# Performance work log

Measured on AMD Instinct MI355X. Metric: run time of the kernel, lower is better.

Reference implementation:

```python
import jax, jax.numpy as jnp
import numpy as np

BN_EPS = 1e-5

def _proj(x, w):
    # 1x1x1 conv, bias=False: pure channel contraction. x: [B,C,T,H,W], w: [O,C]
    return jnp.einsum('bcthw,oc->bothw', x, w)

def _maxpool222(x):
    # MaxPool3d(kernel=2, stride=2); dims are divisible by 2.
    B, C, T, H, W = x.shape
    return x.reshape(B, C, T // 2, 2, H // 2, 2, W // 2, 2).max(axis=(3, 5, 7))

def setup_inputs() -> dict:
    key = jax.random.key(0)
    ks = jax.random.split(key, 5)
    C, Ci = 256, 128
    x = jax.random.normal(ks[0], (4, C, 16, 28, 28), dtype=jnp.float32)
    sc = 1.0 / np.sqrt(C)
    theta_w = jax.random.normal(ks[1], (Ci, C), dtype=jnp.float32) * sc
    phi_w = jax.random.normal(ks[2], (Ci, C), dtype=jnp.float32) * sc
    g_w = jax.random.normal(ks[3], (Ci, C), dtype=jnp.float32) * sc
    z_w = jax.random.normal(ks[4], (C, Ci), dtype=jnp.float32) * (1.0 / np.sqrt(Ci))
    bn_gamma = jnp.ones((C,), dtype=jnp.float32)
    bn_beta = jnp.zeros((C,), dtype=jnp.float32)
    return {"x": x, "theta_w": theta_w, "phi_w": phi_w, "g_w": g_w,
            "z_w": z_w, "bn_gamma": bn_gamma, "bn_beta": bn_beta}

def reference(x, theta_w, phi_w, g_w, z_w, bn_gamma, bn_beta):
    B, C, T, H, W = x.shape
    Ci = theta_w.shape[0]
    N = T * H * W
    theta = _proj(x, theta_w).reshape(B, Ci, N)          # [B,Ci,N]
    phi = _maxpool222(_proj(x, phi_w))                   # [B,Ci,T/2,H/2,W/2]
    g = _maxpool222(_proj(x, g_w))
    Np = phi.shape[2] * phi.shape[3] * phi.shape[4]
    phi = phi.reshape(B, Ci, Np)                         # [B,Ci,Np]
    g = g.reshape(B, Ci, Np)
    attn = jnp.einsum('bcn,bcm->bnm', theta, phi)        # [B,N,Np]
    attn = jax.nn.softmax(attn, axis=-1)
    y = jnp.einsum('bnm,bcm->bcn', attn, g)              # [B,Ci,N]
    y = y.reshape(B, Ci, T, H, W)
    z = _proj(y, z_w)                                    # [B,C,T,H,W]
    # BatchNorm3d in training mode: batch stats over (B,T,H,W), biased var
    mean = z.mean(axis=(0, 2, 3, 4), keepdims=True)
    var = z.var(axis=(0, 2, 3, 4), keepdims=True)
    zn = (z - mean) * jax.lax.rsqrt(var + BN_EPS)
    zn = zn * bn_gamma[None, :, None, None, None] + bn_beta[None, :, None, None, None]
    return x + zn
```

## Files before the change

### kernel.cpp

```cpp
#include <hip/hip_runtime.h>
#include <stdint.h>

#define B_   4
#define C_   256
#define CI_  128
#define T_   16
#define H_   28
#define W_   28
#define HW_  784
#define N_   12544
#define TP_  8
#define HP_  14
#define WP_  14
#define NP_  1568
#define NP2_ 1600
#define NT_  196
#define NT2_ 98
#define NBLK_ 784
#define NBLK2_ 392
#define KVB_ 32
#define NKT_ 49

typedef __attribute__((ext_vector_type(8))) __bf16 bf16x8;
typedef __attribute__((ext_vector_type(4))) float  f32x4;

#define MFMA(a,b,c) __builtin_amdgcn_mfma_f32_16x16x32_bf16(a,b,c,0,0,0)

__device__ __forceinline__ void split_bf16(float f, __bf16& hi, __bf16& lo){
  hi = (__bf16)f;
  lo = (__bf16)(f - (float)hi);
}

__device__ __forceinline__ uint32_t pack2(float a, float b){
  union { __bf16 h; unsigned short s; } ua, ub;
  ua.h = (__bf16)a; ub.h = (__bf16)b;
  return (uint32_t)ua.s | ((uint32_t)ub.s << 16);
}

__device__ __forceinline__ void gload_lds16(const void* g, void* l){
  __builtin_amdgcn_global_load_lds((const __attribute__((address_space(1))) void*)g,
                                   (__attribute__((address_space(3))) void*)l, 16, 0, 0);
}

__global__ __launch_bounds__(256) void k_wconv(const float* __restrict__ wt, const float* __restrict__ wp,
                       const float* __restrict__ wg, const float* __restrict__ zw,
                       __bf16* __restrict__ wth, __bf16* __restrict__ wtl,
                       __bf16* __restrict__ wph, __bf16* __restrict__ wpl,
                       __bf16* __restrict__ wgh, __bf16* __restrict__ wgl,
                       __bf16* __restrict__ zwh, __bf16* __restrict__ zwl){
  int i = blockIdx.x*256 + threadIdx.x;
  if (i < 32768){
    __bf16 h, lo;
    split_bf16(wt[i], h, lo); wth[i]=h; wtl[i]=lo;
    split_bf16(wp[i], h, lo); wph[i]=h; wpl[i]=lo;
    split_bf16(wg[i], h, lo); wgh[i]=h; wgl[i]=lo;
    split_bf16(zw[i], h, lo); zwh[i]=h; zwl[i]=lo;
  }
}

__global__ __launch_bounds__(256,4) void k_proj3(const float* __restrict__ x,
                        const __bf16* __restrict__ wth, const __bf16* __restrict__ wtl,
                        const __bf16* __restrict__ wph, const __bf16* __restrict__ wpl,
                        const __bf16* __restrict__ wgh, const __bf16* __restrict__ wgl,
                        __bf16* __restrict__ th_hi, __bf16* __restrict__ th_lo,
                        float* __restrict__ phf32, __bf16* __restrict__ ggf){
  __shared__ char wbuf[2][16384];
  int wg = blockIdx.x;
  int nt = wg % NT_; int b = wg/NT_;
  int n0 = nt*64;
  int tid = threadIdx.x; int w = tid>>6; int l = tid&63; int lr = l&15; int lg = l>>4;
  int nrow = 16*w + lr;
  const float* xb = x + (size_t)b*C_*N_ + (n0 + nrow);
  bf16x8 Ah[8], Al[8];
  #pragma unroll
  for (int ks=0; ks<8; ++ks){
    #pragma unroll
    for (int j=0;j<8;++j){
      float v = xb[(size_t)(32*ks + 8*lg + j)*N_];
      __bf16 hi, lo; split_bf16(v, hi, lo);
      Ah[ks][j] = hi; Al[ks][j] = lo;
    }
  }
  int sp_part[4]; int sp_rowc[4]; int sp_off[4];
  #pragma unroll
  for (int i=0;i<4;++i){
    int p = i*4096 + tid*16;
    sp_part[i] = p>>13;
    int row = (p>>9)&15;
    int colb = p & 511;
    sp_rowc[i] = row*C_ + ((colb ^ ((row&7)<<4)) >> 1);
    sp_off[i] = i*4096 + w*1024;
  }
  #pragma unroll
  for (int i=0;i<4;++i){
    const __bf16* src = (sp_part[i] ? wtl : wth) + sp_rowc[i];
    gload_lds16(src, &wbuf[0][sp_off[i]]);
  }
  __syncthreads();

  size_t obase = ((size_t)(b*N_ + n0))*CI_;
  int cur = 0;
  for (int pair=0; pair<24; ++pair){
    int p = pair>>3, ot = pair&7;
    if (pair < 23){
      int pn = pair+1, p2 = pn>>3, ot2 = pn&7;
      const __bf16* bh = (p2==0) ? wth : ((p2==1) ? wph : wgh);
      const __bf16* bl = (p2==0) ? wtl : ((p2==1) ? wpl : wgl);
      #pragma unroll
      for (int i=0;i<4;++i){
        const __bf16* src = (sp_part[i] ? bl : bh) + (size_t)(16*ot2)*C_ + sp_rowc[i];
        gload_lds16(src, &wbuf[cur^1][sp_off[i]]);
      }
    }
    const char* wb = wbuf[cur];
    f32x4 aHH={0.f,0.f,0.f,0.f}, aLH={0.f,0.f,0.f,0.f}, aHL={0.f,0.f,0.f,0.f};
    int swz = (lr&7)<<4;
    #pragma unroll
    for (int ks=0; ks<8; ++ks){
      int off = lr*512 + ((ks*64 + lg*16) ^ swz);
      bf16x8 Bh = *(const bf16x8*)(wb + off);
      bf16x8 Bl = *(const bf16x8*)(wb + 8192 + off);
      aHH = MFMA(Ah[ks], Bh, aHH);
      aLH = MFMA(Al[ks], Bh, aLH);
      aHL = MFMA(Ah[ks], Bl, aHL);
    }
    f32x4 acc = aHH + aLH + aHL;
    if (p == 0){
      #pragma unroll
      for (int r=0;r<4;++r){
        int n = 16*w + 4*lg + r;
        __bf16 hi, lo; split_bf16(acc[r], hi, lo);
        th_hi[obase + (size_t)n*CI_ + 16*ot + lr] = hi;
        th_lo[obase + (size_t)n*CI_ + 16*ot + lr] = lo;
      }
    } else if (p == 1){
      #pragma unroll
      for (int r=0;r<4;++r){
        int n = 16*w + 4*lg + r;
        phf32[obase + (size_t)n*CI_ + 16*ot + lr] = acc[r];
      }
    } else {
      #pragma unroll
      for (int r=0;r<4;++r){
        int n = 16*w + 4*lg + r;
        ggf[obase + (size_t)n*CI_ + 16*ot + lr] = (__bf16)acc[r];
      }
    }
    __syncthreads();
    cur ^= 1;
  }
}

__global__ __launch_bounds__(256) void k_pool(const float* __restrict__ phf32, const __bf16* __restrict__ ggf,
                       __bf16* __restrict__ phph, __bf16* __restrict__ phpl,
                       __bf16* __restrict__ ggp){
  int idx = blockIdx.x*256 + threadIdx.x;
  if (idx >= B_*NP2_*16) return;
  int c8 = idx & 15;
  int m  = (idx>>4) % NP2_;
  int b  = idx / (16*NP2_);
  if (m >= NP_){
    bf16x8 zv;
    #pragma unroll
    for (int j=0;j<8;++j) zv[j] = (__bf16)0.f;
    *(bf16x8*)(phph + ((size_t)(b*NP2_ + m))*CI_ + c8*8) = zv;
    *(bf16x8*)(phpl + ((size_t)(b*NP2_ + m))*CI_ + c8*8) = zv;
    #pragma unroll
    for (int j=0;j<8;++j) ggp[((size_t)(b*CI_ + c8*8 + j))*NP2_ + m] = (__bf16)0.f;
    return;
  }
  int tp = m/(HP_*WP_), hp = (m/WP_)%HP_, wq = m%WP_;
  int t0 = tp*2, h0 = hp*2, w0 = wq*2;
  const float*  pb = phf32 + ((size_t)b*N_)*CI_ + c8*8;
  const __bf16* gb = ggf   + ((size_t)b*N_)*CI_ + c8*8;
  float mp[8], mg[8];
  #pragma unroll
  for (int j=0;j<8;++j){ mp[j] = -3e38f; mg[j] = -3e38f; }
  #pragma unroll
  for (int dt=0; dt<2; ++dt)
  #pragma unroll
  for (int dh=0; dh<2; ++dh)
  #pragma unroll
  for (int dw=0; dw<2; ++dw){
    int n = (t0+dt)*HW_ + (h0+dh)*W_ + (w0+dw);
    f32x4 p0 = *(const f32x4*)(pb + (size_t)n*CI_);
    f32x4 p1 = *(const f32x4*)(pb + (size_t)n*CI_ + 4);
    bf16x8 vg = *(const bf16x8*)(gb + (size_t)n*CI_);
    #pragma unroll
    for (int j=0;j<4;++j){ mp[j] = fmaxf(mp[j], p0[j]); mp[4+j] = fmaxf(mp[4+j], p1[j]); }
    #pragma unroll
    for (int j=0;j<8;++j){ mg[j] = fmaxf(mg[j], (float)vg[j]); }
  }
  bf16x8 oh, ol, og;
  #pragma unroll
  for (int j=0;j<8;++j){
    __bf16 hi, lo;
    split_bf16(mp[j], hi, lo);
    oh[j] = hi; ol[j] = lo;
    og[j] = (__bf16)mg[j];
  }
  *(bf16x8*)(phph + ((size_t)(b*NP2_ + m))*CI_ + c8*8) = oh;
  *(bf16x8*)(phpl + ((size_t)(b*NP2_ + m))*CI_ + c8*8) = ol;
  #pragma unroll
  for (int j=0;j<8;++j) ggp[((size_t)(b*CI_ + c8*8 + j))*NP2_ + m] = og[j];
}

__global__ __launch_bounds__(256) void k_phmean1(const __bf16* __restrict__ phph, const __bf16* __restrict__ phpl,
                         float* __restrict__ pph){
  __shared__ float part[2][128];
  int blk = blockIdx.x;
  int b = blk >> 3, g = blk & 7;
  int tid = threadIdx.x;
  int c = tid & 127, mo = tid >> 7;
  const __bf16* ph = phph + (size_t)b*NP2_*CI_ + c;
  const __bf16* pl = phpl + (size_t)b*NP2_*CI_ + c;
  float s = 0.f;
  for (int k=0; k<98; ++k){
    int m = g + 8*(2*k + mo);
    s += (float)ph[(size_t)m*CI_] + (float)pl[(size_t)m*CI_];
  }
  part[mo][c] = s;
  __syncthreads();
  if (tid < 128) pph[(size_t)blk*128 + tid] = part[0][tid] + part[1][tid];
}

__global__ __launch_bounds__(256) void k_phmean2(const float* __restrict__ pph, float* __restrict__ phmean){
  int t = blockIdx.x*256 + threadIdx.x;
  if (t >= B_*CI_) return;
  int b = t >> 7, c = t & 127;
  float s = 0.f;
  #pragma unroll
  for (int g=0; g<8; ++g) s += pph[(size_t)(b*8+g)*128 + c];
  phmean[b*CI_ + c] = s * (1.0f/(float)NP_);
}

__global__ __launch_bounds__(256,2) void k_attn(const __bf16* __restrict__ th_hi, const __bf16* __restrict__ th_lo,
                       const __bf16* __restrict__ phph, const __bf16* __restrict__ phpl,
                       const __bf16* __restrict__ ggp, const float* __restrict__ phmean,
                       __bf16* __restrict__ y){
  __shared__ char sbuf[2][24576];
  __shared__ float estp[128][2];
  __shared__ float est[128];
  int wg = blockIdx.x;
  int nt = wg % NT2_; int b = wg/NT2_;
  int n0 = nt*128;
  int tid = threadIdx.x; int w = tid>>6; int l = tid&63; int lr = l&15; int lg = l>>4;
  const __bf16* phb = phph + (size_t)b*NP2_*CI_;
  const __bf16* plb = phpl + (size_t)b*NP2_*CI_;
  const __bf16* ggb = ggp + (size_t)b*CI_*NP2_;

  {
    int row = tid >> 1, q = tid & 1;
    const __bf16* rh = th_hi + ((size_t)(b*N_ + n0 + row))*CI_ + 64*q;
    const __bf16* rl = th_lo + ((size_t)(b*N_ + n0 + row))*CI_ + 64*q;
    const float* pm = phmean + b*CI_ + 64*q;
    float sacc = 0.f;
    #pragma unroll
    for (int j=0;j<8;++j){
      bf16x8 vh = *(const bf16x8*)(rh + 8*j);
      bf16x8 vl = *(const bf16x8*)(rl + 8*j);
      f32x4 p0 = *(const f32x4*)(pm + 8*j);
      f32x4 p1 = *(const f32x4*)(pm + 8*j + 4);
      #pragma unroll
      for (int k=0;k<4;++k){
        sacc += ((float)vh[k]   + (float)vl[k]  )*p0[k];
        sacc += ((float)vh[4+k] + (float)vl[4+k])*p1[k];
      }
    }
    estp[row][q] = sacc;
  }
  const __bf16* sptr[6]; int sstr[6]; int soff[6];
  #pragma unroll
  for (int jj=0; jj<6; ++jj){
    int j = w*6 + jj;
    int p = j*1024 + l*16;
    int reg = p >> 13;
    int e = p & 8191;
    if (reg < 2){
      int m = e >> 8;
      int chb = (e & 255) ^ ((m & 7) << 4);
      const __bf16* base = (reg==0 ? phb : plb);
      sptr[jj] = base + (size_t)m*CI_ + (chb>>1);
      sstr[jj] = KVB_*CI_;
    } else {
      int c = e >> 6;
      int chb = (e & 63) ^ (((c >> 1) & 3) << 4);
      sptr[jj] = ggb + (size_t)c*NP2_ + (chb>>1);
      sstr[jj] = KVB_;
    }
    soff[jj] = j*1024;
  }
  __syncthreads();
  if (tid < 128) est[tid] = estp[tid][0]+estp[tid][1];

  bf16x8 Ah[2][4], Al[2][4];
  #pragma unroll
  for (int cg=0; cg<2; ++cg){
    size_t tb = ((size_t)(b*N_ + n0 + 32*w + 16*cg))*CI_ + (size_t)lr*CI_;
    #pragma unroll
    for (int ks=0; ks<4; ++ks){
      Ah[cg][ks] = *(const bf16x8*)(th_hi + tb + 32*ks + 8*lg);
      Al[cg][ks] = *(const bf16x8*)(th_lo + tb + 32*ks + 8*lg);
    }
  }
  f32x4 yacc0[8], yacc1[8];
  #pragma unroll
  for (int ct=0; ct<8; ++ct){ yacc0[ct] = (f32x4){0.f,0.f,0.f,0.f}; yacc1[ct] = (f32x4){0.f,0.f,0.f,0.f}; }
  float psum0 = 0.f, psum1 = 0.f;
  __syncthreads();
  float estl0 = est[32*w + lr];
  float estl1 = est[32*w + 16 + lr];

  #pragma unroll
  for (int jj=0; jj<6; ++jj) gload_lds16(sptr[jj], &sbuf[0][soff[jj]]);
  __syncthreads();

  int s1 = lr + (((2*lg)  )&3)*16;
  int s2 = lr + (((2*lg+1))&3)*16;
  bool hi2 = (lg >= 2);

  int cur = 0;
  for (int t=0; t<NKT_; ++t){
    if (t < NKT_-1){
      #pragma unroll
      for (int jj=0; jj<6; ++jj)
        gload_lds16(sptr[jj] + (size_t)(t+1)*sstr[jj], &sbuf[cur^1][soff[jj]]);
    }
    const char* pb_ = sbuf[cur];
    uint32_t qa00, qa01, qa10, qa11, qb00, qb01, qb10, qb11;
    #pragma unroll
    for (int mt=0; mt<2; ++mt){
      f32x4 aHH0={0.f,0.f,0.f,0.f}, aLH0={0.f,0.f,0.f,0.f}, aHL0={0.f,0.f,0.f,0.f};
      f32x4 aHH1={0.f,0.f,0.f,0.f}, aLH1={0.f,0.f,0.f,0.f}, aHL1={0.f,0.f,0.f,0.f};
      int mrow = 16*mt + lr;
      int swz = (mrow&7)<<4;
      #pragma unroll
      for (int ks=0; ks<4; ++ks){
        int off = mrow*256 + ((64*ks + 16*lg) ^ swz);
        bf16x8 Bh = *(const bf16x8*)(pb_ + off);
        bf16x8 Bl = *(const bf16x8*)(pb_ + 8192 + off);
        aHH0 = MFMA(Bh, Ah[0][ks], aHH0);
        aLH0 = MFMA(Bh, Al[0][ks], aLH0);
        aHL0 = MFMA(Bl, Ah[0][ks], aHL0);
        aHH1 = MFMA(Bh, Ah[1][ks], aHH1);
        aLH1 = MFMA(Bh, Al[1][ks], aLH1);
        aHL1 = MFMA(Bl, Ah[1][ks], aHL1);
      }
      f32x4 sv0 = aHH0 + aLH0 + aHL0;
      f32x4 sv1 = aHH1 + aLH1 + aHL1;
      float p00 = __expf(sv0[0]-estl0), p01 = __expf(sv0[1]-estl0);
      float p02 = __expf(sv0[2]-estl0), p03 = __expf(sv0[3]-estl0);
      float p10 = __expf(sv1[0]-estl1), p11 = __expf(sv1[1]-estl1);
      float p12 = __expf(sv1[2]-estl1), p13 = __expf(sv1[3]-estl1);
      psum0 += (p00 + p01) + (p02 + p03);
      psum1 += (p10 + p11) + (p12 + p13);
      uint32_t da0 = pack2(p00,p01), da1 = pack2(p02,p03);
      uint32_t db0 = pack2(p10,p11), db1 = pack2(p12,p13);
      if (mt == 0){ qa00 = da0; qa01 = da1; qb00 = db0; qb01 = db1; }
      else        { qa10 = da0; qa11 = da1; qb10 = db0; qb11 = db1; }
    }
    uint32_t ba00 = __shfl(qa00, s1, 64), ba10 = __shfl(qa10, s1, 64);
    uint32_t ba01 = __shfl(qa01, s1, 64), ba11 = __shfl(qa11, s1, 64);
    uint32_t ca00 = __shfl(qa00, s2, 64), ca10 = __shfl(qa10, s2, 64);
    uint32_t ca01 = __shfl(qa01, s2, 64), ca11 = __shfl(qa11, s2, 64);
    union { uint32_t u[4]; bf16x8 v; } pa0;
    pa0.u[0] = hi2 ? ba10 : ba00;
    pa0.u[1] = hi2 ? ba11 : ba01;
    pa0.u[2] = hi2 ? ca10 : ca00;
    pa0.u[3] = hi2 ? ca11 : ca01;
    uint32_t bb00 = __shfl(qb00, s1, 64), bb10 = __shfl(qb10, s1, 64);
    uint32_t bb01 = __shfl(qb01, s1, 64), bb11 = __shfl(qb11, s1, 64);
    uint32_t cb00 = __shfl(qb00, s2, 64), cb10 = __shfl(qb10, s2, 64);
    uint32_t cb01 = __shfl(qb01, s2, 64), cb11 = __shfl(qb11, s2, 64);
    union { uint32_t u[4]; bf16x8 v; } pa1;
    pa1.u[0] = hi2 ? bb10 : bb00;
    pa1.u[1] = hi2 ? bb11 : bb01;
    pa1.u[2] = hi2 ? cb10 : cb00;
    pa1.u[3] = hi2 ? cb11 : cb01;
    #pragma unroll
    for (int ct=0; ct<8; ++ct){
      int c = 16*ct + lr;
      int goff = 16384 + c*64 + ((16*lg) ^ (((c>>1)&3)<<4));
      bf16x8 Gf = *(const bf16x8*)(pb_ + goff);
      yacc0[ct] = MFMA(pa0.v, Gf, yacc0[ct]);
      yacc1[ct] = MFMA(pa1.v, Gf, yacc1[ct]);
    }
    __syncthreads();
    cur ^= 1;
  }
  float rs0 = psum0;
  rs0 += __shfl_xor(rs0, 16, 64); rs0 += __shfl_xor(rs0, 32, 64);
  float rs1 = psum1;
  rs1 += __shfl_xor(rs1, 16, 64); rs1 += __shfl_xor(rs1, 32, 64);
  float inv0 = 1.0f / rs0, inv1 = 1.0f / rs1;
  float ivr0[4], ivr1[4];
  #pragma unroll
  for (int r=0; r<4; ++r){
    ivr0[r] = __shfl(inv0, 4*lg + r, 64);
    ivr1[r] = __shfl(inv1, 4*lg + r, 64);
  }
  __bf16* yb0 = y + ((size_t)(b*N_ + n0 + 32*w))*CI_;
  __bf16* yb1 = y + ((size_t)(b*N_ + n0 + 32*w + 16))*CI_;
  #pragma unroll
  for (int ct=0; ct<8; ++ct){
    #pragma unroll
    for (int r=0;r<4;++r){
      yb0[(size_t)(4*lg+r)*CI_ + 16*ct + lr] = (__bf16)(yacc0[ct][r] * ivr0[r]);
      yb1[(size_t)(4*lg+r)*CI_ + 16*ct + lr] = (__bf16)(yacc1[ct][r] * ivr1[r]);
    }
  }
}

__global__ __launch_bounds__(256,3) void k_zproj(const __bf16* __restrict__ y,
                        const __bf16* __restrict__ zwh, const __bf16* __restrict__ zwl,
                        __bf16* __restrict__ z, float* __restrict__ pS, float* __restrict__ pQ){
  __shared__ float zt[64][68];
  __shared__ float red[4][256][2];
  __shared__ char wbuf[2][8192];
  int wg = blockIdx.x; int nt = wg % NT_; int b = wg/NT_; int n0 = nt*64;
  int tid = threadIdx.x; int w = tid>>6; int l = tid&63; int lr = l&15; int lg = l>>4;
  const __bf16* yb = y + ((size_t)(b*N_ + n0 + 16*w))*CI_ + (size_t)lr*CI_;
  bf16x8 Ay[4];
  #pragma unroll
  for (int ks=0;ks<4;++ks) Ay[ks] = *(const bf16x8*)(yb + 32*ks + 8*lg);
  int sp_part[2]; int sp_rowc[2]; int sp_off[2];
  #pragma unroll
  for (int i=0;i<2;++i){
    int p = i*4096 + tid*16;
    sp_part[i] = p>>12;
    int row = (p>>8)&15;
    int colb = p & 255;
    sp_rowc[i] = row*CI_ + ((colb ^ ((row&7)<<4)) >> 1);
    sp_off[i] = i*4096 + w*1024;
  }
  #pragma unroll
  for (int i=0;i<2;++i){
    const __bf16* src = (sp_part[i] ? zwl : zwh) + sp_rowc[i];
    gload_lds16(src, &wbuf[0][sp_off[i]]);
  }
  __syncthreads();

  __bf16* zb = z + (size_t)b*C_*N_ + n0;
  int cur = 0;
  for (int og=0; og<4; ++og){
    #pragma unroll
    for (int oi=0; oi<4; ++oi){
      int ot = og*4 + oi;
      if (ot < 15){
        #pragma unroll
        for (int i=0;i<2;++i){
          const __bf16* src = (sp_part[i] ? zwl : zwh) + (size_t)(16*(ot+1))*CI_ + sp_rowc[i];
          gload_lds16(src, &wbuf[cur^1][sp_off[i]]);
        }
      }
      const char* wb = wbuf[cur];
      f32x4 aHH = {0.f,0.f,0.f,0.f}, aHL = {0.f,0.f,0.f,0.f};
      int swz = (lr&7)<<4;
      #pragma unroll
      for (int ks=0;ks<4;++ks){
        int off = lr*256 + ((ks*64 + lg*16) ^ swz);
        bf16x8 Bh = *(const bf16x8*)(wb + off);
        bf16x8 Bl = *(const bf16x8*)(wb + 4096 + off);
        aHH = MFMA(Ay[ks], Bh, aHH);
        aHL = MFMA(Ay[ks], Bl, aHL);
      }
      f32x4 acc = aHH + aHL;
      float s1=0.f, s2=0.f;
      #pragma unroll
      for (int r=0;r<4;++r){
        float v = acc[r];
        int nl = 16*w + 4*lg + r;
        zt[16*oi+lr][nl] = v;
        s1 += v; s2 += v*v;
      }
      s1 += __shfl_xor(s1,16,64); s1 += __shfl_xor(s1,32,64);
      s2 += __shfl_xor(s2,16,64); s2 += __shfl_xor(s2,32,64);
      if (lg==0){ red[w][16*ot+lr][0] = s1; red[w][16*ot+lr][1] = s2; }
      if (oi < 3){ __syncthreads(); cur ^= 1; }
    }
    __syncthreads();
    #pragma unroll
    for (int it=0; it<2; ++it){
      int idx = it*256 + tid;
      int ol = idx>>3, cc = idx&7;
      f32x4 v0 = *(const f32x4*)(&zt[ol][cc*8]);
      f32x4 v1 = *(const f32x4*)(&zt[ol][cc*8+4]);
      bf16x8 o8;
      #pragma unroll
      for (int j=0;j<4;++j){ o8[j] = (__bf16)v0[j]; o8[4+j] = (__bf16)v1[j]; }
      *(bf16x8*)(zb + (size_t)(og*64 + ol)*N_ + cc*8) = o8;
    }
    __syncthreads();
    cur ^= 1;
  }
  float t1 = red[0][tid][0]+red[1][tid][0]+red[2][tid][0]+red[3][tid][0];
  float t2 = red[0][tid][1]+red[1][tid][1]+red[2][tid][1]+red[3][tid][1];
  pS[(size_t)wg*256 + tid] = t1;
  pQ[(size_t)wg*256 + tid] = t2;
}

__global__ __launch_bounds__(256) void k_stats(const float* __restrict__ pS, const float* __restrict__ pQ,
                        const float* __restrict__ gamma, const float* __restrict__ beta,
                        float* __restrict__ coef){
  int o = blockIdx.x; int t = threadIdx.x;
  float s=0.f, q=0.f;
  for (int i=t; i<NBLK_; i+=256){ s += pS[(size_t)i*256+o]; q += pQ[(size_t)i*256+o]; }
  __shared__ float rs[4], rq[4];
  #pragma unroll
  for (int sh=32; sh; sh>>=1){ s += __shfl_down(s,sh,64); q += __shfl_down(q,sh,64); }
  int w = t>>6;
  if ((t&63)==0){ rs[w]=s; rq[w]=q; }
  __syncthreads();
  if (t==0){
    s = rs[0]+rs[1]+rs[2]+rs[3]; q = rq[0]+rq[1]+rq[2]+rq[3];
    float inv = 1.0f/(float)(B_*N_);
    float mean = s*inv, var = q*inv - mean*mean;
    float a = gamma[o]*rsqrtf(var + 1e-5f);
    coef[o] = a; coef[256+o] = beta[o] - mean*a;
  }
}

__global__ __launch_bounds__(256) void k_final(const float* __restrict__ x, const __bf16* __restrict__ z,
                        const float* __restrict__ coef, float* __restrict__ out){
  uint32_t i = blockIdx.x*256 + threadIdx.x;
  uint32_t e0 = i*8u;
  if (e0 >= (uint32_t)(B_*C_*N_)) return;
  int o = (int)((e0 / (uint32_t)N_) % (uint32_t)C_);
  float a = coef[o], b2 = coef[256+o];
  bf16x8 zv = *(const bf16x8*)(z + e0);
  f32x4 x0 = *(const f32x4*)(x + e0);
  f32x4 x1 = *(const f32x4*)(x + e0 + 4);
  f32x4 r0, r1;
  #pragma unroll
  for (int j=0;j<4;++j){
    r0[j] = x0[j] + (float)zv[j]*a + b2;
    r1[j] = x1[j] + (float)zv[4+j]*a + b2;
  }
  *(f32x4*)(out + e0) = r0;
  *(f32x4*)(out + e0 + 4) = r1;
}

extern "C" void kernel_launch(void* const* d_in, const int* in_sizes, int n_in,
                              void* d_out, int out_size, void* d_ws, size_t ws_size,
                              hipStream_t stream){
  const float* x     = (const float*)d_in[0];
  const float* wt    = (const float*)d_in[1];
  const float* wp    = (const float*)d_in[2];
  const float* wg    = (const float*)d_in[3];
  const float* zw    = (const float*)d_in[4];
  const float* gamma = (const float*)d_in[5];
  const float* beta  = (const float*)d_in[6];
  float* out = (float*)d_out;
  char* ws = (char*)d_ws;
  size_t off = 0;
  auto alloc = [&](size_t bytes)->void*{ void* p = ws + off; off = (off + bytes + 255) & ~(size_t)255; return p; };
  __bf16* y    = (__bf16*)alloc((size_t)B_*N_*CI_*2);
  float*  phf32= (float*)alloc((size_t)B_*N_*CI_*4);
  __bf16* ggf  = (__bf16*)alloc((size_t)B_*N_*CI_*2);
  __bf16* th_hi= (__bf16*)alloc((size_t)B_*N_*CI_*2);
  __bf16* th_lo= (__bf16*)alloc((size_t)B_*N_*CI_*2);
  __bf16* wth  = (__bf16*)alloc(32768*2);
  __bf16* wtl  = (__bf16*)alloc(32768*2);
  __bf16* wph  = (__bf16*)alloc(32768*2);
  __bf16* wpl  = (__bf16*)alloc(32768*2);
  __bf16* wgh  = (__bf16*)alloc(32768*2);
  __bf16* wgl  = (__bf16*)alloc(32768*2);
  __bf16* zwh  = (__bf16*)alloc(32768*2);
  __bf16* zwl  = (__bf16*)alloc(32768*2);
  __bf16* phph = (__bf16*)alloc((size_t)B_*NP2_*CI_*2);
  __bf16* phpl = (__bf16*)alloc((size_t)B_*NP2_*CI_*2);
  __bf16* ggp  = (__bf16*)alloc((size_t)B_*CI_*NP2_*2);
  float*  pS   = (float*)alloc((size_t)NBLK_*256*4);
  float*  pQ   = (float*)alloc((size_t)NBLK_*256*4);
  float*  coef = (float*)alloc(512*4);
  float*  phmean = (float*)alloc(B_*CI_*4);
  float*  pph  = (float*)alloc((size_t)B_*8*128*4);
  __bf16* z = (__bf16*)phf32;

  k_wconv<<<128, 256, 0, stream>>>(wt, wp, wg, zw, wth, wtl, wph, wpl, wgh, wgl, zwh, zwl);
  k_proj3<<<NBLK_, 256, 0, stream>>>(x, wth, wtl, wph, wpl, wgh, wgl, th_hi, th_lo, phf32, ggf);
  k_pool<<<(B_*NP2_*16 + 255)/256, 256, 0, stream>>>(phf32, ggf, phph, phpl, ggp);
  k_phmean1<<<B_*8, 256, 0, stream>>>(phph, phpl, pph);
  k_phmean2<<<2, 256, 0, stream>>>(pph, phmean);
  k_attn<<<NBLK2_, 256, 0, stream>>>(th_hi, th_lo, phph, phpl, ggp, phmean, y);
  k_zproj<<<NBLK_, 256, 0, stream>>>(y, zwh, zwl, z, pS, pQ);
  k_stats<<<256, 256, 0, stream>>>(pS, pQ, gamma, beta, coef);
  k_final<<<(B_*C_*N_/8 + 255)/256, 256, 0, stream>>>(x, z, coef, out);
}
```

Measured before the change: 225.3 us.

## Fuse phi-mean partial sums into pool, fold log2e into theta, trim g-proj MFMAs

```diff
diff --git a/kernel.cpp b/kernel.cpp
--- a/kernel.cpp
+++ b/kernel.cpp
@@ -20,6 +20,7 @@
 #define NBLK2_ 392
 #define KVB_ 32
 #define NKT_ 49
+#define LOG2E_ 1.4426950408889634f
 
 typedef __attribute__((ext_vector_type(8))) __bf16 bf16x8;
 typedef __attribute__((ext_vector_type(4))) float  f32x4;
@@ -115,21 +116,32 @@
     const char* wb = wbuf[cur];
     f32x4 aHH={0.f,0.f,0.f,0.f}, aLH={0.f,0.f,0.f,0.f}, aHL={0.f,0.f,0.f,0.f};
     int swz = (lr&7)<<4;
-    #pragma unroll
-    for (int ks=0; ks<8; ++ks){
-      int off = lr*512 + ((ks*64 + lg*16) ^ swz);
-      bf16x8 Bh = *(const bf16x8*)(wb + off);
-      bf16x8 Bl = *(const bf16x8*)(wb + 8192 + off);
-      aHH = MFMA(Ah[ks], Bh, aHH);
-      aLH = MFMA(Al[ks], Bh, aLH);
-      aHL = MFMA(Ah[ks], Bl, aHL);
+    if (p < 2){
+      #pragma unroll
+      for (int ks=0; ks<8; ++ks){
+        int off = lr*512 + ((ks*64 + lg*16) ^ swz);
+        bf16x8 Bh = *(const bf16x8*)(wb + off);
+        bf16x8 Bl = *(const bf16x8*)(wb + 8192 + off);
+        aHH = MFMA(Ah[ks], Bh, aHH);
+        aLH = MFMA(Al[ks], Bh, aLH);
+        aHL = MFMA(Ah[ks], Bl, aHL);
+      }
+    } else {
+      #pragma unroll
+      for (int ks=0; ks<8; ++ks){
+        int off = lr*512 + ((ks*64 + lg*16) ^ swz);
+        bf16x8 Bh = *(const bf16x8*)(wb + off);
+        aHH = MFMA(Ah[ks], Bh, aHH);
+        aLH = MFMA(Al[ks], Bh, aLH);
+      }
     }
     f32x4 acc = aHH + aLH + aHL;
     if (p == 0){
       #pragma unroll
       for (int r=0;r<4;++r){
         int n = 16*w + 4*lg + r;
-        __bf16 hi, lo; split_bf16(acc[r], hi, lo);
+        float sv = acc[r] * LOG2E_;
+        __bf16 hi, lo; split_bf16(sv, hi, lo);
         th_hi[obase + (size_t)n*CI_ + 16*ot + lr] = hi;
         th_lo[obase + (size_t)n*CI_ + 16*ot + lr] = lo;
       }
@@ -153,43 +165,40 @@
 
 __global__ __launch_bounds__(256) void k_pool(const float* __restrict__ phf32, const __bf16* __restrict__ ggf,
                        __bf16* __restrict__ phph, __bf16* __restrict__ phpl,
-                       __bf16* __restrict__ ggp){
-  int idx = blockIdx.x*256 + threadIdx.x;
-  if (idx >= B_*NP2_*16) return;
+                       __bf16* __restrict__ ggp, float* __restrict__ pph){
+  __shared__ float red[16][128];
+  int blk = blockIdx.x;
+  int tid = threadIdx.x;
+  int idx = blk*256 + tid;
   int c8 = idx & 15;
   int m  = (idx>>4) % NP2_;
   int b  = idx / (16*NP2_);
-  if (m >= NP_){
-    bf16x8 zv;
-    #pragma unroll
-    for (int j=0;j<8;++j) zv[j] = (__bf16)0.f;
-    *(bf16x8*)(phph + ((size_t)(b*NP2_ + m))*CI_ + c8*8) = zv;
-    *(bf16x8*)(phpl + ((size_t)(b*NP2_ + m))*CI_ + c8*8) = zv;
-    #pragma unroll
-    for (int j=0;j<8;++j) ggp[((size_t)(b*CI_ + c8*8 + j))*NP2_ + m] = (__bf16)0.f;
-    return;
-  }
-  int tp = m/(HP_*WP_), hp = (m/WP_)%HP_, wq = m%WP_;
-  int t0 = tp*2, h0 = hp*2, w0 = wq*2;
-  const float*  pb = phf32 + ((size_t)b*N_)*CI_ + c8*8;
-  const __bf16* gb = ggf   + ((size_t)b*N_)*CI_ + c8*8;
+  bool valid = (m < NP_);
   float mp[8], mg[8];
   #pragma unroll
-  for (int j=0;j<8;++j){ mp[j] = -3e38f; mg[j] = -3e38f; }
-  #pragma unroll
-  for (int dt=0; dt<2; ++dt)
-  #pragma unroll
-  for (int dh=0; dh<2; ++dh)
-  #pragma unroll
-  for (int dw=0; dw<2; ++dw){
-    int n = (t0+dt)*HW_ + (h0+dh)*W_ + (w0+dw);
-    f32x4 p0 = *(const f32x4*)(pb + (size_t)n*CI_);
-    f32x4 p1 = *(const f32x4*)(pb + (size_t)n*CI_ + 4);
-    bf16x8 vg = *(const bf16x8*)(gb + (size_t)n*CI_);
-    #pragma unroll
-    for (int j=0;j<4;++j){ mp[j] = fmaxf(mp[j], p0[j]); mp[4+j] = fmaxf(mp[4+j], p1[j]); }
-    #pragma unroll
-    for (int j=0;j<8;++j){ mg[j] = fmaxf(mg[j], (float)vg[j]); }
+  for (int j=0;j<8;++j){ mp[j] = 0.f; mg[j] = 0.f; }
+  if (valid){
+    #pragma unroll
+    for (int j=0;j<8;++j){ mp[j] = -3e38f; mg[j] = -3e38f; }
+    int tp = m/(HP_*WP_), hp = (m/WP_)%HP_, wq = m%WP_;
+    int t0 = tp*2, h0 = hp*2, w0 = wq*2;
+    const float*  pb = phf32 + ((size_t)b*N_)*CI_ + c8*8;
+    const __bf16* gb = ggf   + ((size_t)b*N_)*CI_ + c8*8;
+    #pragma unroll
+    for (int dt=0; dt<2; ++dt)
+    #pragma unroll
+    for (int dh=0; dh<2; ++dh)
+    #pragma unroll
+    for (int dw=0; dw<2; ++dw){
+      int n = (t0+dt)*HW_ + (h0+dh)*W_ + (w0+dw);
+      f32x4 p0 = *(const f32x4*)(pb + (size_t)n*CI_);
+      f32x4 p1 = *(const f32x4*)(pb + (size_t)n*CI_ + 4);
+      bf16x8 vg = *(const bf16x8*)(gb + (size_t)n*CI_);
+      #pragma unroll
+      for (int j=0;j<4;++j){ mp[j] = fmaxf(mp[j], p0[j]); mp[4+j] = fmaxf(mp[4+j], p1[j]); }
+      #pragma unroll
+      for (int j=0;j<8;++j){ mg[j] = fmaxf(mg[j], (float)vg[j]); }
+    }
   }
   bf16x8 oh, ol, og;
   #pragma unroll
@@ -203,25 +212,16 @@
   *(bf16x8*)(phpl + ((size_t)(b*NP2_ + m))*CI_ + c8*8) = ol;
   #pragma unroll
   for (int j=0;j<8;++j) ggp[((size_t)(b*CI_ + c8*8 + j))*NP2_ + m] = og[j];
-}
-
-__global__ __launch_bounds__(256) void k_phmean1(const __bf16* __restrict__ phph, const __bf16* __restrict__ phpl,
-                         float* __restrict__ pph){
-  __shared__ float part[2][128];
-  int blk = blockIdx.x;
-  int b = blk >> 3, g = blk & 7;
-  int tid = threadIdx.x;
-  int c = tid & 127, mo = tid >> 7;
-  const __bf16* ph = phph + (size_t)b*NP2_*CI_ + c;
-  const __bf16* pl = phpl + (size_t)b*NP2_*CI_ + c;
-  float s = 0.f;
-  for (int k=0; k<98; ++k){
-    int m = g + 8*(2*k + mo);
-    s += (float)ph[(size_t)m*CI_] + (float)pl[(size_t)m*CI_];
-  }
-  part[mo][c] = s;
-  __syncthreads();
-  if (tid < 128) pph[(size_t)blk*128 + tid] = part[0][tid] + part[1][tid];
+  int ms = tid >> 4;
+  #pragma unroll
+  for (int j=0;j<8;++j) red[ms][c8*8 + j] = mp[j];
+  __syncthreads();
+  if (tid < 128){
+    float s = 0.f;
+    #pragma unroll
+    for (int k=0;k<16;++k) s += red[k][tid];
+    pph[(size_t)blk*128 + tid] = s;
+  }
 }
 
 __global__ __launch_bounds__(256) void k_phmean2(const float* __restrict__ pph, float* __restrict__ phmean){
@@ -229,8 +229,7 @@
   if (t >= B_*CI_) return;
   int b = t >> 7, c = t & 127;
   float s = 0.f;
-  #pragma unroll
-  for (int g=0; g<8; ++g) s += pph[(size_t)(b*8+g)*128 + c];
+  for (int k=0; k<100; ++k) s += pph[(size_t)(b*100+k)*128 + c];
   phmean[b*CI_ + c] = s * (1.0f/(float)NP_);
 }
 
@@ -348,10 +347,10 @@
       }
       f32x4 sv0 = aHH0 + aLH0 + aHL0;
       f32x4 sv1 = aHH1 + aLH1 + aHL1;
-      float p00 = __expf(sv0[0]-estl0), p01 = __expf(sv0[1]-estl0);
-      float p02 = __expf(sv0[2]-estl0), p03 = __expf(sv0[3]-estl0);
-      float p10 = __expf(sv1[0]-estl1), p11 = __expf(sv1[1]-estl1);
-      float p12 = __expf(sv1[2]-estl1), p13 = __expf(sv1[3]-estl1);
+      float p00 = exp2f(sv0[0]-estl0), p01 = exp2f(sv0[1]-estl0);
+      float p02 = exp2f(sv0[2]-estl0), p03 = exp2f(sv0[3]-estl0);
+      float p10 = exp2f(sv1[0]-estl1), p11 = exp2f(sv1[1]-estl1);
+      float p12 = exp2f(sv1[2]-estl1), p13 = exp2f(sv1[3]-estl1);
       psum0 += (p00 + p01) + (p02 + p03);
       psum1 += (p10 + p11) + (p12 + p13);
       uint32_t da0 = pack2(p00,p01), da1 = pack2(p02,p03);
@@ -574,13 +573,12 @@
   float*  pQ   = (float*)alloc((size_t)NBLK_*256*4);
   float*  coef = (float*)alloc(512*4);
   float*  phmean = (float*)alloc(B_*CI_*4);
-  float*  pph  = (float*)alloc((size_t)B_*8*128*4);
+  float*  pph  = (float*)alloc((size_t)400*128*4);
   __bf16* z = (__bf16*)phf32;
 
   k_wconv<<<128, 256, 0, stream>>>(wt, wp, wg, zw, wth, wtl, wph, wpl, wgh, wgl, zwh, zwl);
   k_proj3<<<NBLK_, 256, 0, stream>>>(x, wth, wtl, wph, wpl, wgh, wgl, th_hi, th_lo, phf32, ggf);
-  k_pool<<<(B_*NP2_*16 + 255)/256, 256, 0, stream>>>(phf32, ggf, phph, phpl, ggp);
-  k_phmean1<<<B_*8, 256, 0, stream>>>(phph, phpl, pph);
+  k_pool<<<400, 256, 0, stream>>>(phf32, ggf, phph, phpl, ggp, pph);
   k_phmean2<<<2, 256, 0, stream>>>(pph, phmean);
   k_attn<<<NBLK2_, 256, 0, stream>>>(th_hi, th_lo, phph, phpl, ggp, phmean, y);
   k_zproj<<<NBLK_, 256, 0, stream>>>(y, zwh, zwl, z, pS, pQ);
```

Measured after the change: 227.1 us. No clear change (+0.8%).
